# Optimization experiments

Hardware: AMD Instinct MI355X
Metric: run time of the kernel (lower is better)

The kernel has to match this reference:

```python
import jax, jax.numpy as jnp
import numpy as np

T, H, E, I = 512, 2048, 8, 4096
W_SCALE = 0.02  # keep activations numerically sane with randn weights


def setup_inputs() -> dict:
    key = jax.random.key(0)
    k_x, k_r, k_w1, k_w3, k_w2 = jax.random.split(key, 5)
    x = jax.random.normal(k_x, (T, H), dtype=jnp.float32)
    router_logits = jax.random.normal(k_r, (T, E), dtype=jnp.float32)
    w1 = jax.random.normal(k_w1, (E, I, H), dtype=jnp.float32) * W_SCALE  # gate proj (silu branch)
    w3 = jax.random.normal(k_w3, (E, I, H), dtype=jnp.float32) * W_SCALE  # up proj
    w2 = jax.random.normal(k_w2, (E, H, I), dtype=jnp.float32) * W_SCALE  # down proj
    return {"x": x, "router_logits": router_logits, "w1": w1, "w3": w3, "w2": w2}


def reference(x, router_logits, w1, w3, w2):
    # Llama4 routing: top-1 expert, router weight = sigmoid(top logit),
    # applied on the INPUT (apply_router_weight_on_input=True).
    top_logit = jnp.max(router_logits, axis=-1)          # [T]
    expert_idx = jnp.argmax(router_logits, axis=-1)      # [T] int
    scale = jax.nn.sigmoid(top_logit)                    # [T]
    xs = x * scale[:, None]                              # [T, H]

    # Grouped SwiGLU experts (dense over E, combined with one-hot select;
    # faithful to fused grouped-GEMM math of FusedMoE).
    gate = jnp.einsum('th,eih->eti', xs, w1)             # [E, T, I]
    up = jnp.einsum('th,eih->eti', xs, w3)               # [E, T, I]
    h = jax.nn.silu(gate) * up                           # [E, T, I]
    y = jnp.einsum('eti,ehi->eth', h, w2)                # [E, T, H]

    onehot = jax.nn.one_hot(expert_idx, E, dtype=x.dtype)  # [T, E]
    out = jnp.einsum('te,eth->th', onehot, y)            # [T, H]
    return out
```

## Files before the change

kernel.cpp:

```cpp
#include <hip/hip_runtime.h>

#define T_TOK 512
#define HDIM 2048
#define NEXP 8
#define IDIM 4096

#define BM 128
#define BK 64
#define G1_BN 32
#define G2_BN 16

typedef float f32x4 __attribute__((ext_vector_type(4)));
typedef __bf16 bf16x8 __attribute__((ext_vector_type(8)));
typedef unsigned short ushort8 __attribute__((ext_vector_type(8)));

static __device__ __forceinline__ unsigned short f2bf(float f) {
    unsigned int u = __float_as_uint(f);
    u = (u + 0x7fffu + ((u >> 16) & 1u)) >> 16;
    return (unsigned short)u;
}

static __device__ __forceinline__ void gload_lds16(const void* g, void* l) {
    auto gp = reinterpret_cast<const unsigned int __attribute__((address_space(1)))*>(
        reinterpret_cast<unsigned long long>(g));
    auto lp = reinterpret_cast<unsigned int __attribute__((address_space(3)))*>(
        static_cast<unsigned int>(reinterpret_cast<unsigned long long>(l)));
    __builtin_amdgcn_global_load_lds(gp, lp, 16, 0, 0);
}

__global__ void k_route(const float* __restrict__ logits,
                        int* __restrict__ off, int* __restrict__ tok,
                        float* __restrict__ scale) {
    __shared__ int cnt[NEXP], cur[NEXP];
    const int t = threadIdx.x;
    if (t < NEXP) cnt[t] = 0;
    __syncthreads();
    float m = logits[t * NEXP];
    int a = 0;
#pragma unroll
    for (int j = 1; j < NEXP; ++j) {
        float v = logits[t * NEXP + j];
        if (v > m) { m = v; a = j; }
    }
    scale[t] = 1.f / (1.f + __expf(-m));
    atomicAdd(&cnt[a], 1);
    __syncthreads();
    if (t == 0) {
        int o = 0;
        for (int e = 0; e < NEXP; ++e) { off[e] = o; cur[e] = o; o += cnt[e]; }
        off[NEXP] = o;
    }
    __syncthreads();
    int r = atomicAdd(&cur[a], 1);
    tok[r] = t;
}

__global__ void k_gather(const float* __restrict__ x, const int* __restrict__ tok,
                         const float* __restrict__ scale,
                         unsigned short* __restrict__ xs) {
    const int pos = blockIdx.x;
    const int t = tok[pos];
    const float s = scale[t];
    const int c = threadIdx.x * 8;
    const float4* src = (const float4*)(x + (size_t)t * HDIM + c);
    float4 v0 = src[0], v1 = src[1];
    ushort8 o;
    o[0] = f2bf(v0.x * s); o[1] = f2bf(v0.y * s);
    o[2] = f2bf(v0.z * s); o[3] = f2bf(v0.w * s);
    o[4] = f2bf(v1.x * s); o[5] = f2bf(v1.y * s);
    o[6] = f2bf(v1.z * s); o[7] = f2bf(v1.w * s);
    *(ushort8*)(xs + (size_t)pos * HDIM + c) = o;
}

__global__ void __launch_bounds__(256, 4)
k_moe1(const unsigned short* __restrict__ xs,
       const float* __restrict__ w1,
       const float* __restrict__ w3,
       const int* __restrict__ off,
       unsigned short* __restrict__ hbuf) {
    __shared__ unsigned short sA[BM * BK];
    __shared__ float sB1[G1_BN * BK];
    __shared__ float sB3[G1_BN * BK];

    const int tid = threadIdx.x;
    const int w = tid >> 6, l = tid & 63;
    const int e = blockIdx.x >> 7;
    const int n0 = (blockIdx.x & 127) * G1_BN;
    const int pos_beg = off[e], pos_end = off[e + 1];

    const char* bw1 = (const char*)(w1 + (size_t)e * IDIM * HDIM + (size_t)n0 * HDIM);
    const char* bw3 = (const char*)(w3 + (size_t)e * IDIM * HDIM + (size_t)n0 * HDIM);

    const int a_row = w * 8 + (l >> 3);
    const int a_cb  = ((l & 7) ^ (l >> 3)) << 4;
    const int b_row = w * 4 + (l >> 4);
    const int b_cb  = ((l & 15) << 4) ^ (((w * 4 + (l >> 4)) & 7) << 5);

    for (int m0 = pos_beg; m0 < pos_end; m0 += BM) {
        f32x4 zero = {0.f, 0.f, 0.f, 0.f};
        f32x4 accG[2][2], accU[2][2];
#pragma unroll
        for (int i = 0; i < 2; ++i)
#pragma unroll
            for (int j = 0; j < 2; ++j) { accG[i][j] = zero; accU[i][j] = zero; }

#pragma unroll 1
        for (int ks = 0; ks < HDIM / BK; ++ks) {
            const int k0 = ks * BK;
#pragma unroll
            for (int j = 0; j < 4; ++j) {
                const int o = j * 4096 + w * 1024;
                int gr = m0 + j * 32 + a_row; gr = gr < T_TOK ? gr : T_TOK - 1;
                gload_lds16((const char*)xs + (size_t)gr * (HDIM * 2) + k0 * 2 + a_cb,
                            (char*)sA + o);
            }
#pragma unroll
            for (int j = 0; j < 2; ++j) {
                const int o = j * 4096 + w * 1024;
                const size_t roff = (size_t)(j * 16 + b_row) * (HDIM * 4) + k0 * 4 + b_cb;
                gload_lds16(bw1 + roff, (char*)sB1 + o);
                gload_lds16(bw3 + roff, (char*)sB3 + o);
            }
            asm volatile("s_waitcnt vmcnt(0)" ::: "memory");
            __syncthreads();

#pragma unroll
            for (int kk = 0; kk < 2; ++kk) {
                bf16x8 a[2];
#pragma unroll
                for (int fm = 0; fm < 2; ++fm) {
                    const int row = w * 32 + fm * 16 + (l & 15);
                    const int kb = (kk * 64 + ((l >> 4) << 4)) ^ ((l & 7) << 4);
                    a[fm] = *(const bf16x8*)((const char*)sA + row * 128 + kb);
                }
#pragma unroll
                for (int fn = 0; fn < 2; ++fn) {
                    const int row = fn * 16 + (l & 15);
                    const int kb = (kk * 128 + ((l >> 4) << 5)) ^ ((l & 7) << 5);
                    const char* p1 = (const char*)sB1 + row * 256 + kb;
                    const char* p3 = (const char*)sB3 + row * 256 + kb;
                    f32x4 g0 = *(const f32x4*)p1, g1 = *(const f32x4*)(p1 + 16);
                    f32x4 u0 = *(const f32x4*)p3, u1 = *(const f32x4*)(p3 + 16);
                    bf16x8 bg, bu;
#pragma unroll
                    for (int q = 0; q < 4; ++q) {
                        bg[q] = (__bf16)g0[q]; bg[q + 4] = (__bf16)g1[q];
                        bu[q] = (__bf16)u0[q]; bu[q + 4] = (__bf16)u1[q];
                    }
#pragma unroll
                    for (int fm = 0; fm < 2; ++fm) {
                        accG[fm][fn] = __builtin_amdgcn_mfma_f32_16x16x32_bf16(
                            a[fm], bg, accG[fm][fn], 0, 0, 0);
                        accU[fm][fn] = __builtin_amdgcn_mfma_f32_16x16x32_bf16(
                            a[fm], bu, accU[fm][fn], 0, 0, 0);
                    }
                }
            }
            __syncthreads();
        }

#pragma unroll
        for (int fm = 0; fm < 2; ++fm)
#pragma unroll
            for (int fn = 0; fn < 2; ++fn)
#pragma unroll
                for (int r = 0; r < 4; ++r) {
                    const int pos = m0 + w * 32 + fm * 16 + ((l >> 4) << 2) + r;
                    if (pos < pos_end) {
                        const float gv = accG[fm][fn][r];
                        const float uv = accU[fm][fn][r];
                        const float hv = gv / (1.f + __expf(-gv)) * uv;
                        hbuf[(size_t)pos * IDIM + n0 + fn * 16 + (l & 15)] = f2bf(hv);
                    }
                }
    }
}

__global__ void __launch_bounds__(256, 4)
k_moe2(const unsigned short* __restrict__ hbuf,
       const float* __restrict__ w2,
       const int* __restrict__ off,
       const int* __restrict__ tok,
       float* __restrict__ out) {
    __shared__ unsigned short sA[BM * BK];
    __shared__ float sB[G2_BN * BK];

    const int tid = threadIdx.x;
    const int w = tid >> 6, l = tid & 63;
    const int e = blockIdx.x >> 7;
    const int n0 = (blockIdx.x & 127) * G2_BN;
    const int pos_beg = off[e], pos_end = off[e + 1];
    const char* bw2 = (const char*)(w2 + (size_t)e * HDIM * IDIM + (size_t)n0 * IDIM);

    const int a_row = w * 8 + (l >> 3);
    const int a_cb  = ((l & 7) ^ (l >> 3)) << 4;
    const int b_row = w * 4 + (l >> 4);
    const int b_cb  = ((l & 15) << 4) ^ (((w * 4 + (l >> 4)) & 7) << 5);

    for (int m0 = pos_beg; m0 < pos_end; m0 += BM) {
        f32x4 zero = {0.f, 0.f, 0.f, 0.f};
        f32x4 acc[2];
        acc[0] = zero; acc[1] = zero;

#pragma unroll 1
        for (int ks = 0; ks < IDIM / BK; ++ks) {
            const int k0 = ks * BK;
#pragma unroll
            for (int j = 0; j < 4; ++j) {
                const int o = j * 4096 + w * 1024;
                int gr = m0 + j * 32 + a_row; gr = gr < T_TOK ? gr : T_TOK - 1;
                gload_lds16((const char*)hbuf + (size_t)gr * (IDIM * 2) + k0 * 2 + a_cb,
                            (char*)sA + o);
            }
            {
                const int o = w * 1024;
                gload_lds16(bw2 + (size_t)b_row * (IDIM * 4) + k0 * 4 + b_cb,
                            (char*)sB + o);
            }
            asm volatile("s_waitcnt vmcnt(0)" ::: "memory");
            __syncthreads();

#pragma unroll
            for (int kk = 0; kk < 2; ++kk) {
                const int brow = l & 15;
                const int bkb = (kk * 128 + ((l >> 4) << 5)) ^ ((l & 7) << 5);
                const char* pb = (const char*)sB + brow * 256 + bkb;
                f32x4 b0 = *(const f32x4*)pb, b1 = *(const f32x4*)(pb + 16);
                bf16x8 bb;
#pragma unroll
                for (int q = 0; q < 4; ++q) {
                    bb[q] = (__bf16)b0[q]; bb[q + 4] = (__bf16)b1[q];
                }
#pragma unroll
                for (int fm = 0; fm < 2; ++fm) {
                    const int row = w * 32 + fm * 16 + (l & 15);
                    const int kb = (kk * 64 + ((l >> 4) << 4)) ^ ((l & 7) << 4);
                    bf16x8 a = *(const bf16x8*)((const char*)sA + row * 128 + kb);
                    acc[fm] = __builtin_amdgcn_mfma_f32_16x16x32_bf16(a, bb, acc[fm], 0, 0, 0);
                }
            }
            __syncthreads();
        }

#pragma unroll
        for (int fm = 0; fm < 2; ++fm)
#pragma unroll
            for (int r = 0; r < 4; ++r) {
                const int pos = m0 + w * 32 + fm * 16 + ((l >> 4) << 2) + r;
                if (pos < pos_end) {
                    const int t = tok[pos];
                    out[(size_t)t * HDIM + n0 + (l & 15)] = acc[fm][r];
                }
            }
    }
}

extern "C" void kernel_launch(void* const* d_in, const int* in_sizes, int n_in,
                              void* d_out, int out_size, void* d_ws, size_t ws_size,
                              hipStream_t stream) {
    const float* x      = (const float*)d_in[0];
    const float* logits = (const float*)d_in[1];
    const float* w1     = (const float*)d_in[2];
    const float* w3     = (const float*)d_in[3];
    const float* w2     = (const float*)d_in[4];
    float* out = (float*)d_out;

    char* ws = (char*)d_ws;
    int* off   = (int*)ws;
    int* tok   = (int*)(ws + 64);
    float* scl = (float*)(ws + 64 + 2048);
    unsigned short* xs   = (unsigned short*)(ws + 8192);
    unsigned short* hbuf = (unsigned short*)(ws + 8192 + (size_t)T_TOK * HDIM * 2);

    k_route<<<1, T_TOK, 0, stream>>>(logits, off, tok, scl);
    k_gather<<<T_TOK, 256, 0, stream>>>(x, tok, scl, xs);
    k_moe1<<<NEXP * (IDIM / G1_BN), 256, 0, stream>>>(xs, w1, w3, off, hbuf);
    k_moe2<<<NEXP * (HDIM / G2_BN), 256, 0, stream>>>(hbuf, w2, off, tok, out);
}
```

Measured before the change: 216.2 us.

## Double-buffer LDS tiles in both MoE GEMM kernels to overlap loads with MFMA

```diff
diff --git a/kernel.cpp b/kernel.cpp
--- a/kernel.cpp
+++ b/kernel.cpp
@@ -72,15 +72,13 @@
     *(ushort8*)(xs + (size_t)pos * HDIM + c) = o;
 }
 
-__global__ void __launch_bounds__(256, 4)
+__global__ void __launch_bounds__(256, 2)
 k_moe1(const unsigned short* __restrict__ xs,
        const float* __restrict__ w1,
        const float* __restrict__ w3,
        const int* __restrict__ off,
        unsigned short* __restrict__ hbuf) {
-    __shared__ unsigned short sA[BM * BK];
-    __shared__ float sB1[G1_BN * BK];
-    __shared__ float sB3[G1_BN * BK];
+    __shared__ char smem[65536];
 
     const int tid = threadIdx.x;
     const int w = tid >> 6, l = tid & 63;
@@ -104,26 +102,35 @@
 #pragma unroll
             for (int j = 0; j < 2; ++j) { accG[i][j] = zero; accU[i][j] = zero; }
 
+        auto stage = [&](int buf, int ks) {
+            const int k0 = ks * BK;
+#pragma unroll
+            for (int j = 0; j < 4; ++j) {
+                const int o = buf * 16384 + j * 4096 + w * 1024;
+                int gr = m0 + j * 32 + a_row; gr = gr < T_TOK ? gr : T_TOK - 1;
+                gload_lds16((const char*)xs + (size_t)gr * (HDIM * 2) + k0 * 2 + a_cb,
+                            smem + o);
+            }
+#pragma unroll
+            for (int j = 0; j < 2; ++j) {
+                const size_t roff = (size_t)(j * 16 + b_row) * (HDIM * 4) + k0 * 4 + b_cb;
+                gload_lds16(bw1 + roff, smem + 32768 + buf * 8192 + j * 4096 + w * 1024);
+                gload_lds16(bw3 + roff, smem + 49152 + buf * 8192 + j * 4096 + w * 1024);
+            }
+        };
+
+        stage(0, 0);
+        asm volatile("s_waitcnt vmcnt(0)" ::: "memory");
+        __syncthreads();
+
 #pragma unroll 1
         for (int ks = 0; ks < HDIM / BK; ++ks) {
-            const int k0 = ks * BK;
-#pragma unroll
-            for (int j = 0; j < 4; ++j) {
-                const int o = j * 4096 + w * 1024;
-                int gr = m0 + j * 32 + a_row; gr = gr < T_TOK ? gr : T_TOK - 1;
-                gload_lds16((const char*)xs + (size_t)gr * (HDIM * 2) + k0 * 2 + a_cb,
-                            (char*)sA + o);
-            }
-#pragma unroll
-            for (int j = 0; j < 2; ++j) {
-                const int o = j * 4096 + w * 1024;
-                const size_t roff = (size_t)(j * 16 + b_row) * (HDIM * 4) + k0 * 4 + b_cb;
-                gload_lds16(bw1 + roff, (char*)sB1 + o);
-                gload_lds16(bw3 + roff, (char*)sB3 + o);
-            }
-            asm volatile("s_waitcnt vmcnt(0)" ::: "memory");
-            __syncthreads();
-
+            const int cb = ks & 1;
+            if (ks + 1 < HDIM / BK) stage(cb ^ 1, ks + 1);
+
+            const char* cA  = smem + cb * 16384;
+            const char* cB1 = smem + 32768 + cb * 8192;
+            const char* cB3 = smem + 49152 + cb * 8192;
 #pragma unroll
             for (int kk = 0; kk < 2; ++kk) {
                 bf16x8 a[2];
@@ -131,14 +138,14 @@
                 for (int fm = 0; fm < 2; ++fm) {
                     const int row = w * 32 + fm * 16 + (l & 15);
                     const int kb = (kk * 64 + ((l >> 4) << 4)) ^ ((l & 7) << 4);
-                    a[fm] = *(const bf16x8*)((const char*)sA + row * 128 + kb);
+                    a[fm] = *(const bf16x8*)(cA + row * 128 + kb);
                 }
 #pragma unroll
                 for (int fn = 0; fn < 2; ++fn) {
                     const int row = fn * 16 + (l & 15);
                     const int kb = (kk * 128 + ((l >> 4) << 5)) ^ ((l & 7) << 5);
-                    const char* p1 = (const char*)sB1 + row * 256 + kb;
-                    const char* p3 = (const char*)sB3 + row * 256 + kb;
+                    const char* p1 = cB1 + row * 256 + kb;
+                    const char* p3 = cB3 + row * 256 + kb;
                     f32x4 g0 = *(const f32x4*)p1, g1 = *(const f32x4*)(p1 + 16);
                     f32x4 u0 = *(const f32x4*)p3, u1 = *(const f32x4*)(p3 + 16);
                     bf16x8 bg, bu;
@@ -156,6 +163,7 @@
                     }
                 }
             }
+            asm volatile("s_waitcnt vmcnt(0)" ::: "memory");
             __syncthreads();
         }
 
@@ -182,8 +190,7 @@
        const int* __restrict__ off,
        const int* __restrict__ tok,
        float* __restrict__ out) {
-    __shared__ unsigned short sA[BM * BK];
-    __shared__ float sB[G2_BN * BK];
+    __shared__ char smem[40960];
 
     const int tid = threadIdx.x;
     const int w = tid >> 6, l = tid & 63;
@@ -202,29 +209,35 @@
         f32x4 acc[2];
         acc[0] = zero; acc[1] = zero;
 
+        auto stage = [&](int buf, int ks) {
+            const int k0 = ks * BK;
+#pragma unroll
+            for (int j = 0; j < 4; ++j) {
+                const int o = buf * 16384 + j * 4096 + w * 1024;
+                int gr = m0 + j * 32 + a_row; gr = gr < T_TOK ? gr : T_TOK - 1;
+                gload_lds16((const char*)hbuf + (size_t)gr * (IDIM * 2) + k0 * 2 + a_cb,
+                            smem + o);
+            }
+            gload_lds16(bw2 + (size_t)b_row * (IDIM * 4) + k0 * 4 + b_cb,
+                        smem + 32768 + buf * 4096 + w * 1024);
+        };
+
+        stage(0, 0);
+        asm volatile("s_waitcnt vmcnt(0)" ::: "memory");
+        __syncthreads();
+
 #pragma unroll 1
         for (int ks = 0; ks < IDIM / BK; ++ks) {
-            const int k0 = ks * BK;
-#pragma unroll
-            for (int j = 0; j < 4; ++j) {
-                const int o = j * 4096 + w * 1024;
-                int gr = m0 + j * 32 + a_row; gr = gr < T_TOK ? gr : T_TOK - 1;
-                gload_lds16((const char*)hbuf + (size_t)gr * (IDIM * 2) + k0 * 2 + a_cb,
-                            (char*)sA + o);
-            }
-            {
-                const int o = w * 1024;
-                gload_lds16(bw2 + (size_t)b_row * (IDIM * 4) + k0 * 4 + b_cb,
-                            (char*)sB + o);
-            }
-            asm volatile("s_waitcnt vmcnt(0)" ::: "memory");
-            __syncthreads();
-
+            const int cb = ks & 1;
+            if (ks + 1 < IDIM / BK) stage(cb ^ 1, ks + 1);
+
+            const char* cA = smem + cb * 16384;
+            const char* cB = smem + 32768 + cb * 4096;
 #pragma unroll
             for (int kk = 0; kk < 2; ++kk) {
                 const int brow = l & 15;
                 const int bkb = (kk * 128 + ((l >> 4) << 5)) ^ ((l & 7) << 5);
-                const char* pb = (const char*)sB + brow * 256 + bkb;
+                const char* pb = cB + brow * 256 + bkb;
                 f32x4 b0 = *(const f32x4*)pb, b1 = *(const f32x4*)(pb + 16);
                 bf16x8 bb;
 #pragma unroll
@@ -235,10 +248,11 @@
                 for (int fm = 0; fm < 2; ++fm) {
                     const int row = w * 32 + fm * 16 + (l & 15);
                     const int kb = (kk * 64 + ((l >> 4) << 4)) ^ ((l & 7) << 4);
-                    bf16x8 a = *(const bf16x8*)((const char*)sA + row * 128 + kb);
+                    bf16x8 a = *(const bf16x8*)(cA + row * 128 + kb);
                     acc[fm] = __builtin_amdgcn_mfma_f32_16x16x32_bf16(a, bb, acc[fm], 0, 0, 0);
                 }
             }
+            asm volatile("s_waitcnt vmcnt(0)" ::: "memory");
             __syncthreads();
         }
 
```

Measured after the change: 218.8 us. No clear change (+1.2%).
